# Kernel tuning notes

Measured on AMD Instinct MI355X. Metric: run time of the kernel, lower is better.

The kernel has to match this reference:

```python
import jax, jax.numpy as jnp
import numpy as np

EMBED_DIM = 1024
NUM_HEADS = 16
HEAD_DIM = EMBED_DIM // NUM_HEADS
WINDOW = 256
B, S = 2, 2048


def setup_inputs() -> dict:
    key = jax.random.key(0)
    ks = jax.random.split(key, 9)
    sc = 1.0 / np.sqrt(EMBED_DIM)
    inp = {
        "x": jax.random.normal(ks[0], (B, S, EMBED_DIM), dtype=jnp.float32),
        "Wq": jax.random.normal(ks[1], (EMBED_DIM, EMBED_DIM), dtype=jnp.float32) * sc,
        "Wk": jax.random.normal(ks[2], (EMBED_DIM, EMBED_DIM), dtype=jnp.float32) * sc,
        "Wv": jax.random.normal(ks[3], (EMBED_DIM, EMBED_DIM), dtype=jnp.float32) * sc,
        "Wo": jax.random.normal(ks[4], (EMBED_DIM, EMBED_DIM), dtype=jnp.float32) * sc,
        "bq": jax.random.normal(ks[5], (EMBED_DIM,), dtype=jnp.float32) * 0.01,
        "bk": jax.random.normal(ks[6], (EMBED_DIM,), dtype=jnp.float32) * 0.01,
        "bv": jax.random.normal(ks[7], (EMBED_DIM,), dtype=jnp.float32) * 0.01,
        "bo": jax.random.normal(ks[8], (EMBED_DIM,), dtype=jnp.float32) * 0.01,
    }
    return inp


def _sliding_window_mask(seq_len: int) -> jnp.ndarray:
    # True where attention is NOT permitted (future or beyond window)
    idx = jnp.arange(seq_len)
    rel = idx[None, :] - idx[:, None]  # (S, S): key_pos - query_pos
    return (rel > 0) | (rel < -WINDOW)


def reference(x, Wq, Wk, Wv, Wo, bq, bk, bv, bo):
    Bx, Sx, E = x.shape
    H, D = NUM_HEADS, HEAD_DIM
    # projections (torch Linear: y = x @ W.T + b)
    q = (x @ Wq.T + bq).reshape(Bx, Sx, H, D).transpose(0, 2, 1, 3)  # (B,H,S,D)
    k = (x @ Wk.T + bk).reshape(Bx, Sx, H, D).transpose(0, 2, 1, 3)
    v = (x @ Wv.T + bv).reshape(Bx, Sx, H, D).transpose(0, 2, 1, 3)
    q = q * (D ** -0.5)
    attn = jnp.einsum("bhqd,bhkd->bhqk", q, k)  # (B,H,S,S) dense scores
    mask = _sliding_window_mask(Sx)
    attn = jnp.where(mask, -jnp.inf, attn)
    attn = jax.nn.softmax(attn, axis=-1)
    y = jnp.einsum("bhqk,bhkd->bhqd", attn, v)
    y = y.transpose(0, 2, 1, 3).reshape(Bx, Sx, E)
    return y @ Wo.T + bo
```

## Files before the change

### kernel.cpp

```cpp
#include <hip/hip_runtime.h>

#define E_DIM 1024
#define NHEAD 16
#define HDIM 64
#define SEQ 2048
#define NBATCH 2
#define WIN 256
#define MTOK (NBATCH * SEQ)
#define BKT 32
#define NT (E_DIM / BKT)

typedef __attribute__((ext_vector_type(4))) float f32x4;
typedef __attribute__((ext_vector_type(8))) short short8;
typedef __attribute__((ext_vector_type(4))) unsigned short u16x4;

#define AS1 __attribute__((address_space(1)))
#define AS3 __attribute__((address_space(3)))

__device__ __forceinline__ void gll16(const void* g, void* l) {
    __builtin_amdgcn_global_load_lds((const AS1 void*)g, (AS3 void*)l, 16, 0, 0);
}

__device__ __forceinline__ unsigned short f2bf(float f) {
    union { float f; unsigned u; } a; a.f = f;
    unsigned r = a.u + 0x7fffu + ((a.u >> 16) & 1u);
    return (unsigned short)(r >> 16);
}

__global__ __launch_bounds__(256) void conv_f2b(const float* __restrict__ src,
                                                unsigned short* __restrict__ dst, int n4) {
    int i = blockIdx.x * 256 + threadIdx.x;
    int stride = gridDim.x * 256;
    for (; i < n4; i += stride) {
        float4 v = ((const float4*)src)[i];
        u16x4 o;
        o[0] = f2bf(v.x); o[1] = f2bf(v.y); o[2] = f2bf(v.z); o[3] = f2bf(v.w);
        ((u16x4*)dst)[i] = o;
    }
}

__global__ __launch_bounds__(256) void conv_w4(const float* __restrict__ w0, const float* __restrict__ w1,
                                               const float* __restrict__ w2, const float* __restrict__ w3,
                                               unsigned short* __restrict__ o0, unsigned short* __restrict__ o1,
                                               unsigned short* __restrict__ o2, unsigned short* __restrict__ o3) {
    const int m = blockIdx.y;
    const float* src = (m == 0) ? w0 : (m == 1) ? w1 : (m == 2) ? w2 : w3;
    unsigned short* dst = (m == 0) ? o0 : (m == 1) ? o1 : (m == 2) ? o2 : o3;
    int i = blockIdx.x * 256 + threadIdx.x;
    float4 v = ((const float4*)src)[i];
    u16x4 o;
    o[0] = f2bf(v.x); o[1] = f2bf(v.y); o[2] = f2bf(v.z); o[3] = f2bf(v.w);
    ((u16x4*)dst)[i] = o;
}

__global__ __launch_bounds__(512, 2) void gemm8_qkv(const unsigned short* __restrict__ xb,
        const unsigned short* __restrict__ wqb, const unsigned short* __restrict__ wkb,
        const unsigned short* __restrict__ wvb,
        const float* __restrict__ bq, const float* __restrict__ bk, const float* __restrict__ bv,
        unsigned short* __restrict__ qo, unsigned short* __restrict__ ko,
        unsigned short* __restrict__ vTo) {
    __shared__ char lds[131072];
    const int tid = threadIdx.x;
    const int w = tid >> 6, l = tid & 63;
    const int r16 = l & 15, kq = l >> 4;
    const int wm = w >> 2, wn = w & 3;
    const int m0 = blockIdx.x * 256;
    const int by = blockIdx.y;
    const int mat = by >> 2;
    const int nb = (by & 3) * 256;
    const unsigned short* Bw = (mat == 0) ? wqb : (mat == 1) ? wkb : wvb;

    const int srow = tid >> 2;
    const int sslot = tid & 3;
    const int fsw = (srow >> 1) & 3;
    const int gslot = (sslot ^ fsw) * 8;
    const unsigned short* aSrc0 = xb + (size_t)(m0 + srow) * E_DIM + gslot;
    const unsigned short* aSrc1 = aSrc0 + (size_t)128 * E_DIM;
    const unsigned short* bSrc0 = Bw + (size_t)(nb + srow) * E_DIM + gslot;
    const unsigned short* bSrc1 = bSrc0 + (size_t)128 * E_DIM;
    const int dstOff = w * 1024;

#define STAGE_A(t) { char* d_ = lds + ((t) & 3) * 32768 + dstOff; \
                     gll16(aSrc0 + (t) * BKT, d_); gll16(aSrc1 + (t) * BKT, d_ + 8192); }
#define STAGE_B(t) { char* d_ = lds + ((t) & 3) * 32768 + 16384 + dstOff; \
                     gll16(bSrc0 + (t) * BKT, d_); gll16(bSrc1 + (t) * BKT, d_ + 8192); }

    f32x4 acc[8][4];
    #pragma unroll
    for (int m = 0; m < 8; ++m)
        #pragma unroll
        for (int n = 0; n < 4; ++n)
            acc[m][n] = (f32x4){0.f, 0.f, 0.f, 0.f};

    STAGE_A(0); STAGE_B(0); STAGE_A(1); STAGE_B(1);

    const int fs = (r16 >> 1) & 3;
    const int rdoff = (kq ^ fs) * 16;

    for (int t = 0; t < NT; ++t) {
        if (t < NT - 1) { asm volatile("s_waitcnt vmcnt(4)" ::: "memory"); }
        else            { asm volatile("s_waitcnt vmcnt(0)" ::: "memory"); }
        __builtin_amdgcn_sched_barrier(0);
        __builtin_amdgcn_s_barrier();
        __builtin_amdgcn_sched_barrier(0);
        char* la = lds + (t & 3) * 32768;
        char* lb = la + 16384;
        short8 bfr[4], af[4];
        #pragma unroll
        for (int n = 0; n < 4; ++n)
            bfr[n] = *(const short8*)(lb + (wn * 64 + n * 16 + r16) * 64 + rdoff);
        #pragma unroll
        for (int j = 0; j < 4; ++j)
            af[j] = *(const short8*)(la + (wm * 128 + j * 16 + r16) * 64 + rdoff);
        if (t + 2 < NT) STAGE_A(t + 2);
        __builtin_amdgcn_s_barrier();
        __builtin_amdgcn_sched_barrier(0);
        __builtin_amdgcn_s_setprio(1);
        #pragma unroll
        for (int j = 0; j < 4; ++j)
            #pragma unroll
            for (int n = 0; n < 4; ++n)
                acc[j][n] = __builtin_amdgcn_mfma_f32_16x16x32_bf16(af[j], bfr[n], acc[j][n], 0, 0, 0);
        __builtin_amdgcn_s_setprio(0);
        short8 af2[4];
        #pragma unroll
        for (int j = 0; j < 4; ++j)
            af2[j] = *(const short8*)(la + (wm * 128 + (4 + j) * 16 + r16) * 64 + rdoff);
        if (t + 2 < NT) STAGE_B(t + 2);
        __builtin_amdgcn_s_barrier();
        __builtin_amdgcn_sched_barrier(0);
        __builtin_amdgcn_s_setprio(1);
        #pragma unroll
        for (int j = 0; j < 4; ++j)
            #pragma unroll
            for (int n = 0; n < 4; ++n)
                acc[4 + j][n] = __builtin_amdgcn_mfma_f32_16x16x32_bf16(af2[j], bfr[n], acc[4 + j][n], 0, 0, 0);
        __builtin_amdgcn_s_setprio(0);
    }
#undef STAGE_A
#undef STAGE_B

    const float* bias = (mat == 0) ? bq : (mat == 1) ? bk : bv;
    const float scale = (mat == 0) ? 0.125f : 1.0f;
    #pragma unroll
    for (int n = 0; n < 4; ++n) {
        int e = nb + wn * 64 + n * 16 + r16;
        float bb = bias[e];
        int h = e >> 6, d = e & 63;
        #pragma unroll
        for (int m = 0; m < 8; ++m) {
            int tok = m0 + wm * 128 + m * 16 + kq * 4;
            int b = tok >> 11, s = tok & (SEQ - 1);
            if (mat == 2) {
                u16x4 o;
                #pragma unroll
                for (int r = 0; r < 4; ++r) o[r] = f2bf(acc[m][n][r] + bb);
                *(u16x4*)(vTo + ((size_t)(b * NHEAD + h) * HDIM + d) * SEQ + s) = o;
            } else {
                unsigned short* dst = (mat == 0) ? qo : ko;
                #pragma unroll
                for (int r = 0; r < 4; ++r) {
                    float val = (acc[m][n][r] + bb) * scale;
                    dst[((size_t)(b * NHEAD + h) * SEQ + s + r) * HDIM + d] = f2bf(val);
                }
            }
        }
    }
}

__device__ __forceinline__ void gemm_tile(const unsigned short* __restrict__ A,
                                          const unsigned short* __restrict__ Bw,
                                          int m0, int n0,
                                          f32x4 acc[4][4], char* ldsA, char* ldsB) {
    const int t = threadIdx.x;
    const int w = t >> 6, l = t & 63;
    const int r16 = l & 15, kq = l >> 4;
    const int wr = w >> 1, wc = w & 1;
    const int srow = l >> 3, ps = l & 7;

    for (int kt = 0; kt < E_DIM / 64; ++kt) {
        #pragma unroll
        for (int c = 0; c < 4; ++c) {
            int chunk = w * 4 + c;
            int row = chunk * 8 + srow;
            int kslot = ps ^ (row & 7);
            gll16(A  + (size_t)(m0 + row) * E_DIM + kt * 64 + kslot * 8, ldsA + chunk * 1024);
            gll16(Bw + (size_t)(n0 + row) * E_DIM + kt * 64 + kslot * 8, ldsB + chunk * 1024);
        }
        __syncthreads();
        #pragma unroll
        for (int kk = 0; kk < 2; ++kk) {
            short8 af[4], bfr[4];
            #pragma unroll
            for (int m = 0; m < 4; ++m) {
                int rr = wr * 64 + m * 16 + r16;
                int c = kk * 4 + kq;
                af[m] = *(const short8*)(ldsA + rr * 128 + ((c ^ (rr & 7)) * 16));
            }
            #pragma unroll
            for (int n = 0; n < 4; ++n) {
                int rr = wc * 64 + n * 16 + r16;
                int c = kk * 4 + kq;
                bfr[n] = *(const short8*)(ldsB + rr * 128 + ((c ^ (rr & 7)) * 16));
            }
            #pragma unroll
            for (int m = 0; m < 4; ++m)
                #pragma unroll
                for (int n = 0; n < 4; ++n)
                    acc[m][n] = __builtin_amdgcn_mfma_f32_16x16x32_bf16(af[m], bfr[n], acc[m][n], 0, 0, 0);
        }
        __syncthreads();
    }
}

__global__ __launch_bounds__(256) void attn_swa(const unsigned short* __restrict__ q,
                                                const unsigned short* __restrict__ k,
                                                const unsigned short* __restrict__ vT,
                                                unsigned short* __restrict__ y) {
    __shared__ char plds[4 * 4096];
    const int t = threadIdx.x;
    const int w = t >> 6, l = t & 63;
    const int r16 = l & 15, kq = l >> 4;
    const int wid = blockIdx.x * 4 + w;
    const int bh = wid >> 6;
    const int q0 = (wid & 63) * 32;
    const unsigned short* qp = q + (size_t)bh * SEQ * HDIM;
    const unsigned short* kp = k + (size_t)bh * SEQ * HDIM;
    const unsigned short* vp = vT + (size_t)bh * HDIM * SEQ;
    char* pl = plds + w * 4096;

    short8 qf[2][2];
    #pragma unroll
    for (int mf = 0; mf < 2; ++mf) {
        const unsigned short* qr = qp + (q0 + mf * 16 + r16) * HDIM + kq * 8;
        qf[mf][0] = *(const short8*)(qr);
        qf[mf][1] = *(const short8*)(qr + 32);
    }

    f32x4 po[2][4];
    float mrow[2][4], lrow[2][4];
    #pragma unroll
    for (int mf = 0; mf < 2; ++mf) {
        #pragma unroll
        for (int nn = 0; nn < 4; ++nn) po[mf][nn] = (f32x4){0.f, 0.f, 0.f, 0.f};
        #pragma unroll
        for (int r = 0; r < 4; ++r) { mrow[mf][r] = -1e30f; lrow[mf][r] = 0.f; }
    }

    const int kstart = (q0 >= WIN) ? (q0 - WIN) : 0;
    for (int k0 = kstart; k0 <= q0 + 31; k0 += 32) {
        short8 kf[2][2];
        #pragma unroll
        for (int n = 0; n < 2; ++n) {
            const unsigned short* kr = kp + (size_t)(k0 + n * 16 + r16) * HDIM + kq * 8;
            kf[n][0] = *(const short8*)(kr);
            kf[n][1] = *(const short8*)(kr + 32);
        }
        f32x4 sc[2][2];
        #pragma unroll
        for (int mf = 0; mf < 2; ++mf)
            #pragma unroll
            for (int n = 0; n < 2; ++n) {
                f32x4 z = {0.f, 0.f, 0.f, 0.f};
                z = __builtin_amdgcn_mfma_f32_16x16x32_bf16(qf[mf][0], kf[n][0], z, 0, 0, 0);
                sc[mf][n] = __builtin_amdgcn_mfma_f32_16x16x32_bf16(qf[mf][1], kf[n][1], z, 0, 0, 0);
            }
        float tmax[2][4];
        #pragma unroll
        for (int mf = 0; mf < 2; ++mf)
            #pragma unroll
            for (int r = 0; r < 4; ++r) {
                int qrow = q0 + mf * 16 + kq * 4 + r;
                int key0 = k0 + r16;
                int key1 = key0 + 16;
                if (!(key0 <= qrow && key0 >= qrow - WIN)) sc[mf][0][r] = -1e30f;
                if (!(key1 <= qrow && key1 >= qrow - WIN)) sc[mf][1][r] = -1e30f;
                tmax[mf][r] = fmaxf(sc[mf][0][r], sc[mf][1][r]);
            }
        #pragma unroll
        for (int off = 1; off < 16; off <<= 1)
            #pragma unroll
            for (int mf = 0; mf < 2; ++mf)
                #pragma unroll
                for (int r = 0; r < 4; ++r)
                    tmax[mf][r] = fmaxf(tmax[mf][r], __shfl_xor(tmax[mf][r], off));
        float pv[2][2][4], psum[2][4];
        #pragma unroll
        for (int mf = 0; mf < 2; ++mf)
            #pragma unroll
            for (int r = 0; r < 4; ++r) {
                float mnew = fmaxf(mrow[mf][r], tmax[mf][r]);
                float resc = __expf(mrow[mf][r] - mnew);
                mrow[mf][r] = mnew;
                lrow[mf][r] *= resc;
                po[mf][0][r] *= resc; po[mf][1][r] *= resc;
                po[mf][2][r] *= resc; po[mf][3][r] *= resc;
                float p0 = (sc[mf][0][r] > -1e29f) ? __expf(sc[mf][0][r] - mnew) : 0.f;
                float p1 = (sc[mf][1][r] > -1e29f) ? __expf(sc[mf][1][r] - mnew) : 0.f;
                pv[mf][0][r] = p0; pv[mf][1][r] = p1;
                psum[mf][r] = p0 + p1;
            }
        #pragma unroll
        for (int off = 1; off < 16; off <<= 1)
            #pragma unroll
            for (int mf = 0; mf < 2; ++mf)
                #pragma unroll
                for (int r = 0; r < 4; ++r)
                    psum[mf][r] += __shfl_xor(psum[mf][r], off);
        #pragma unroll
        for (int mf = 0; mf < 2; ++mf)
            #pragma unroll
            for (int r = 0; r < 4; ++r) lrow[mf][r] += psum[mf][r];

        #pragma unroll
        for (int mf = 0; mf < 2; ++mf)
            #pragma unroll
            for (int r = 0; r < 4; ++r) {
                int row = kq * 4 + r;
                int c0 = r16 ^ ((row & 7) << 3);
                int c1 = (16 + r16) ^ ((row & 7) << 3);
                *(unsigned short*)(pl + mf * 2048 + row * 128 + c0 * 2) = f2bf(pv[mf][0][r]);
                *(unsigned short*)(pl + mf * 2048 + row * 128 + c1 * 2) = f2bf(pv[mf][1][r]);
            }
        short8 pa[2];
        #pragma unroll
        for (int mf = 0; mf < 2; ++mf)
            pa[mf] = *(const short8*)(pl + mf * 2048 + r16 * 128 + ((kq ^ (r16 & 7)) * 16));
        #pragma unroll
        for (int nn = 0; nn < 4; ++nn) {
            short8 vf = *(const short8*)(vp + (size_t)(nn * 16 + r16) * SEQ + k0 + kq * 8);
            po[0][nn] = __builtin_amdgcn_mfma_f32_16x16x32_bf16(pa[0], vf, po[0][nn], 0, 0, 0);
            po[1][nn] = __builtin_amdgcn_mfma_f32_16x16x32_bf16(pa[1], vf, po[1][nn], 0, 0, 0);
        }
    }

    const int b = bh >> 4, h = bh & 15;
    #pragma unroll
    for (int mf = 0; mf < 2; ++mf)
        #pragma unroll
        for (int nn = 0; nn < 4; ++nn)
            #pragma unroll
            for (int r = 0; r < 4; ++r) {
                int s = q0 + mf * 16 + kq * 4 + r;
                float val = po[mf][nn][r] / lrow[mf][r];
                y[((size_t)(b * SEQ + s)) * E_DIM + h * HDIM + nn * 16 + r16] = f2bf(val);
            }
}

__global__ __launch_bounds__(256) void gemm_out(const unsigned short* __restrict__ yb,
        const unsigned short* __restrict__ wob, const float* __restrict__ bo,
        float* __restrict__ out) {
    __shared__ char lds[32768];
    const int m0 = blockIdx.x * 128;
    const int n0 = blockIdx.y * 128;
    f32x4 acc[4][4];
    #pragma unroll
    for (int m = 0; m < 4; ++m)
        #pragma unroll
        for (int n = 0; n < 4; ++n)
            acc[m][n] = (f32x4){0.f, 0.f, 0.f, 0.f};

    gemm_tile(yb, wob, m0, n0, acc, lds, lds + 16384);

    const int t = threadIdx.x;
    const int w = t >> 6, l = t & 63;
    const int r16 = l & 15, kq = l >> 4;
    const int wr = w >> 1, wc = w & 1;
    #pragma unroll
    for (int n = 0; n < 4; ++n) {
        int e = n0 + wc * 64 + n * 16 + r16;
        float bb = bo[e];
        #pragma unroll
        for (int m = 0; m < 4; ++m) {
            #pragma unroll
            for (int r = 0; r < 4; ++r) {
                int tok = m0 + wr * 64 + m * 16 + kq * 4 + r;
                out[(size_t)tok * E_DIM + e] = acc[m][n][r] + bb;
            }
        }
    }
}

extern "C" void kernel_launch(void* const* d_in, const int* in_sizes, int n_in,
                              void* d_out, int out_size, void* d_ws, size_t ws_size,
                              hipStream_t stream) {
    const float* x  = (const float*)d_in[0];
    const float* Wq = (const float*)d_in[1];
    const float* Wk = (const float*)d_in[2];
    const float* Wv = (const float*)d_in[3];
    const float* Wo = (const float*)d_in[4];
    const float* bq = (const float*)d_in[5];
    const float* bk = (const float*)d_in[6];
    const float* bv = (const float*)d_in[7];
    const float* bo = (const float*)d_in[8];
    float* out = (float*)d_out;

    char* ws = (char*)d_ws;
    unsigned short* xb  = (unsigned short*)(ws);
    unsigned short* wqb = (unsigned short*)(ws + ((size_t)8 << 20));
    unsigned short* wkb = (unsigned short*)(ws + ((size_t)10 << 20));
    unsigned short* wvb = (unsigned short*)(ws + ((size_t)12 << 20));
    unsigned short* wob = (unsigned short*)(ws + ((size_t)14 << 20));
    unsigned short* qw  = (unsigned short*)(ws + ((size_t)16 << 20));
    unsigned short* kw  = (unsigned short*)(ws + ((size_t)24 << 20));
    unsigned short* vTw = (unsigned short*)(ws + ((size_t)40 << 20));
    unsigned short* yw  = (unsigned short*)(ws + ((size_t)48 << 20));

    conv_f2b<<<4096, 256, 0, stream>>>(x, xb, MTOK * E_DIM / 4);
    conv_w4<<<dim3(1024, 4), 256, 0, stream>>>(Wq, Wk, Wv, Wo, wqb, wkb, wvb, wob);

    gemm8_qkv<<<dim3(16, 12), 512, 0, stream>>>(xb, wqb, wkb, wvb, bq, bk, bv, qw, kw, vTw);
    attn_swa<<<512, 256, 0, stream>>>(qw, kw, vTw, yw);
    gemm_out<<<dim3(32, 8), 256, 0, stream>>>(yw, wob, bo, out);
}
```

Baseline: 177.3 us.

## Merge conversion kernels, simplify QKV GEMM loop, pipeline output GEMM

Merges the x and weight fp32-to-bf16 conversion kernels into a single launch with eight segments. The QKV GEMM's main loop now loads all eight A fragments at once and issues both stage loads together, dropping one barrier per iteration. The output projection GEMM gets the same 4-stage global_load_lds pipeline with BK=32, XOR swizzle and 2 blocks per CU. This is meant to cut launch overhead, barrier stalls and exposed load latency, at the cost of more registers held for fragments.

After: 166.1 us. 1.07x faster.

```diff
diff --git a/kernel.cpp b/kernel.cpp
--- a/kernel.cpp
+++ b/kernel.cpp
@@ -27,25 +27,20 @@
     return (unsigned short)(r >> 16);
 }
 
-__global__ __launch_bounds__(256) void conv_f2b(const float* __restrict__ src,
-                                                unsigned short* __restrict__ dst, int n4) {
-    int i = blockIdx.x * 256 + threadIdx.x;
-    int stride = gridDim.x * 256;
-    for (; i < n4; i += stride) {
-        float4 v = ((const float4*)src)[i];
-        u16x4 o;
-        o[0] = f2bf(v.x); o[1] = f2bf(v.y); o[2] = f2bf(v.z); o[3] = f2bf(v.w);
-        ((u16x4*)dst)[i] = o;
-    }
-}
-
-__global__ __launch_bounds__(256) void conv_w4(const float* __restrict__ w0, const float* __restrict__ w1,
-                                               const float* __restrict__ w2, const float* __restrict__ w3,
-                                               unsigned short* __restrict__ o0, unsigned short* __restrict__ o1,
-                                               unsigned short* __restrict__ o2, unsigned short* __restrict__ o3) {
-    const int m = blockIdx.y;
-    const float* src = (m == 0) ? w0 : (m == 1) ? w1 : (m == 2) ? w2 : w3;
-    unsigned short* dst = (m == 0) ? o0 : (m == 1) ? o1 : (m == 2) ? o2 : o3;
+__global__ __launch_bounds__(256) void conv_all(const float* __restrict__ x,
+        const float* __restrict__ w0, const float* __restrict__ w1,
+        const float* __restrict__ w2, const float* __restrict__ w3,
+        unsigned short* __restrict__ xo,
+        unsigned short* __restrict__ o0, unsigned short* __restrict__ o1,
+        unsigned short* __restrict__ o2, unsigned short* __restrict__ o3) {
+    const int seg = blockIdx.y;
+    const float* src;
+    unsigned short* dst;
+    if (seg < 4) { src = x + (size_t)seg * 1048576; dst = xo + (size_t)seg * 1048576; }
+    else {
+        src = (seg == 4) ? w0 : (seg == 5) ? w1 : (seg == 6) ? w2 : w3;
+        dst = (seg == 4) ? o0 : (seg == 5) ? o1 : (seg == 6) ? o2 : o3;
+    }
     int i = blockIdx.x * 256 + threadIdx.x;
     float4 v = ((const float4*)src)[i];
     u16x4 o;
@@ -105,36 +100,20 @@
         __builtin_amdgcn_sched_barrier(0);
         char* la = lds + (t & 3) * 32768;
         char* lb = la + 16384;
-        short8 bfr[4], af[4];
+        short8 bfr[4], af[8];
         #pragma unroll
         for (int n = 0; n < 4; ++n)
             bfr[n] = *(const short8*)(lb + (wn * 64 + n * 16 + r16) * 64 + rdoff);
         #pragma unroll
-        for (int j = 0; j < 4; ++j)
+        for (int j = 0; j < 8; ++j)
             af[j] = *(const short8*)(la + (wm * 128 + j * 16 + r16) * 64 + rdoff);
-        if (t + 2 < NT) STAGE_A(t + 2);
-        __builtin_amdgcn_s_barrier();
-        __builtin_amdgcn_sched_barrier(0);
+        if (t + 2 < NT) { STAGE_A(t + 2); STAGE_B(t + 2); }
         __builtin_amdgcn_s_setprio(1);
         #pragma unroll
-        for (int j = 0; j < 4; ++j)
+        for (int j = 0; j < 8; ++j)
             #pragma unroll
             for (int n = 0; n < 4; ++n)
                 acc[j][n] = __builtin_amdgcn_mfma_f32_16x16x32_bf16(af[j], bfr[n], acc[j][n], 0, 0, 0);
-        __builtin_amdgcn_s_setprio(0);
-        short8 af2[4];
-        #pragma unroll
-        for (int j = 0; j < 4; ++j)
-            af2[j] = *(const short8*)(la + (wm * 128 + (4 + j) * 16 + r16) * 64 + rdoff);
-        if (t + 2 < NT) STAGE_B(t + 2);
-        __builtin_amdgcn_s_barrier();
-        __builtin_amdgcn_sched_barrier(0);
-        __builtin_amdgcn_s_setprio(1);
-        #pragma unroll
-        for (int j = 0; j < 4; ++j)
-            #pragma unroll
-            for (int n = 0; n < 4; ++n)
-                acc[4 + j][n] = __builtin_amdgcn_mfma_f32_16x16x32_bf16(af2[j], bfr[n], acc[4 + j][n], 0, 0, 0);
         __builtin_amdgcn_s_setprio(0);
     }
 #undef STAGE_A
@@ -168,48 +147,83 @@
     }
 }
 
-__device__ __forceinline__ void gemm_tile(const unsigned short* __restrict__ A,
-                                          const unsigned short* __restrict__ Bw,
-                                          int m0, int n0,
-                                          f32x4 acc[4][4], char* ldsA, char* ldsB) {
-    const int t = threadIdx.x;
-    const int w = t >> 6, l = t & 63;
+__global__ __launch_bounds__(256, 2) void gemm_out(const unsigned short* __restrict__ yb,
+        const unsigned short* __restrict__ wob, const float* __restrict__ bo,
+        float* __restrict__ out) {
+    __shared__ char lds[65536];
+    const int tid = threadIdx.x;
+    const int w = tid >> 6, l = tid & 63;
     const int r16 = l & 15, kq = l >> 4;
     const int wr = w >> 1, wc = w & 1;
-    const int srow = l >> 3, ps = l & 7;
-
-    for (int kt = 0; kt < E_DIM / 64; ++kt) {
-        #pragma unroll
-        for (int c = 0; c < 4; ++c) {
-            int chunk = w * 4 + c;
-            int row = chunk * 8 + srow;
-            int kslot = ps ^ (row & 7);
-            gll16(A  + (size_t)(m0 + row) * E_DIM + kt * 64 + kslot * 8, ldsA + chunk * 1024);
-            gll16(Bw + (size_t)(n0 + row) * E_DIM + kt * 64 + kslot * 8, ldsB + chunk * 1024);
+    const int m0 = blockIdx.x * 128;
+    const int n0 = blockIdx.y * 128;
+
+    const int srow = tid >> 2;
+    const int sslot = tid & 3;
+    const int fsw = (srow >> 1) & 3;
+    const int gslot = (sslot ^ fsw) * 8;
+    const unsigned short* aSrc0 = yb + (size_t)(m0 + srow) * E_DIM + gslot;
+    const unsigned short* aSrc1 = aSrc0 + (size_t)64 * E_DIM;
+    const unsigned short* bSrc0 = wob + (size_t)(n0 + srow) * E_DIM + gslot;
+    const unsigned short* bSrc1 = bSrc0 + (size_t)64 * E_DIM;
+    const int dstOff = w * 1024;
+
+#define STAGE_A(t) { char* d_ = lds + ((t) & 3) * 16384 + dstOff; \
+                     gll16(aSrc0 + (t) * BKT, d_); gll16(aSrc1 + (t) * BKT, d_ + 4096); }
+#define STAGE_B(t) { char* d_ = lds + ((t) & 3) * 16384 + 8192 + dstOff; \
+                     gll16(bSrc0 + (t) * BKT, d_); gll16(bSrc1 + (t) * BKT, d_ + 4096); }
+
+    f32x4 acc[4][4];
+    #pragma unroll
+    for (int m = 0; m < 4; ++m)
+        #pragma unroll
+        for (int n = 0; n < 4; ++n)
+            acc[m][n] = (f32x4){0.f, 0.f, 0.f, 0.f};
+
+    STAGE_A(0); STAGE_B(0); STAGE_A(1); STAGE_B(1);
+
+    const int fs = (r16 >> 1) & 3;
+    const int rdoff = (kq ^ fs) * 16;
+
+    for (int t = 0; t < NT; ++t) {
+        if (t < NT - 1) { asm volatile("s_waitcnt vmcnt(4)" ::: "memory"); }
+        else            { asm volatile("s_waitcnt vmcnt(0)" ::: "memory"); }
+        __builtin_amdgcn_sched_barrier(0);
+        __builtin_amdgcn_s_barrier();
+        __builtin_amdgcn_sched_barrier(0);
+        char* la = lds + (t & 3) * 16384;
+        char* lb = la + 8192;
+        short8 bfr[4], af[4];
+        #pragma unroll
+        for (int n = 0; n < 4; ++n)
+            bfr[n] = *(const short8*)(lb + (wc * 64 + n * 16 + r16) * 64 + rdoff);
+        #pragma unroll
+        for (int m = 0; m < 4; ++m)
+            af[m] = *(const short8*)(la + (wr * 64 + m * 16 + r16) * 64 + rdoff);
+        if (t + 2 < NT) { STAGE_A(t + 2); STAGE_B(t + 2); }
+        __builtin_amdgcn_s_setprio(1);
+        #pragma unroll
+        for (int m = 0; m < 4; ++m)
+            #pragma unroll
+            for (int n = 0; n < 4; ++n)
+                acc[m][n] = __builtin_amdgcn_mfma_f32_16x16x32_bf16(af[m], bfr[n], acc[m][n], 0, 0, 0);
+        __builtin_amdgcn_s_setprio(0);
+    }
+#undef STAGE_A
+#undef STAGE_B
+
+    #pragma unroll
+    for (int n = 0; n < 4; ++n) {
+        int e = n0 + wc * 64 + n * 16 + r16;
+        float bb = bo[e];
+        #pragma unroll
+        for (int m = 0; m < 4; ++m) {
+            #pragma unroll
+            for (int r = 0; r < 4; ++r) {
+                int tok = m0 + wr * 64 + m * 16 + kq * 4 + r;
+                out[(size_t)tok * E_DIM + e] = acc[m][n][r] + bb;
+            }
         }
-        __syncthreads();
-        #pragma unroll
-        for (int kk = 0; kk < 2; ++kk) {
-            short8 af[4], bfr[4];
-            #pragma unroll
-            for (int m = 0; m < 4; ++m) {
-                int rr = wr * 64 + m * 16 + r16;
-                int c = kk * 4 + kq;
-                af[m] = *(const short8*)(ldsA + rr * 128 + ((c ^ (rr & 7)) * 16));
-            }
-            #pragma unroll
-            for (int n = 0; n < 4; ++n) {
-                int rr = wc * 64 + n * 16 + r16;
-                int c = kk * 4 + kq;
-                bfr[n] = *(const short8*)(ldsB + rr * 128 + ((c ^ (rr & 7)) * 16));
-            }
-            #pragma unroll
-            for (int m = 0; m < 4; ++m)
-                #pragma unroll
-                for (int n = 0; n < 4; ++n)
-                    acc[m][n] = __builtin_amdgcn_mfma_f32_16x16x32_bf16(af[m], bfr[n], acc[m][n], 0, 0, 0);
-        }
-        __syncthreads();
     }
 }
 
@@ -347,40 +361,6 @@
             }
 }
 
-__global__ __launch_bounds__(256) void gemm_out(const unsigned short* __restrict__ yb,
-        const unsigned short* __restrict__ wob, const float* __restrict__ bo,
-        float* __restrict__ out) {
-    __shared__ char lds[32768];
-    const int m0 = blockIdx.x * 128;
-    const int n0 = blockIdx.y * 128;
-    f32x4 acc[4][4];
-    #pragma unroll
-    for (int m = 0; m < 4; ++m)
-        #pragma unroll
-        for (int n = 0; n < 4; ++n)
-            acc[m][n] = (f32x4){0.f, 0.f, 0.f, 0.f};
-
-    gemm_tile(yb, wob, m0, n0, acc, lds, lds + 16384);
-
-    const int t = threadIdx.x;
-    const int w = t >> 6, l = t & 63;
-    const int r16 = l & 15, kq = l >> 4;
-    const int wr = w >> 1, wc = w & 1;
-    #pragma unroll
-    for (int n = 0; n < 4; ++n) {
-        int e = n0 + wc * 64 + n * 16 + r16;
-        float bb = bo[e];
-        #pragma unroll
-        for (int m = 0; m < 4; ++m) {
-            #pragma unroll
-            for (int r = 0; r < 4; ++r) {
-                int tok = m0 + wr * 64 + m * 16 + kq * 4 + r;
-                out[(size_t)tok * E_DIM + e] = acc[m][n][r] + bb;
-            }
-        }
-    }
-}
-
 extern "C" void kernel_launch(void* const* d_in, const int* in_sizes, int n_in,
                               void* d_out, int out_size, void* d_ws, size_t ws_size,
                               hipStream_t stream) {
@@ -406,8 +386,7 @@
     unsigned short* vTw = (unsigned short*)(ws + ((size_t)40 << 20));
     unsigned short* yw  = (unsigned short*)(ws + ((size_t)48 << 20));
 
-    conv_f2b<<<4096, 256, 0, stream>>>(x, xb, MTOK * E_DIM / 4);
-    conv_w4<<<dim3(1024, 4), 256, 0, stream>>>(Wq, Wk, Wv, Wo, wqb, wkb, wvb, wob);
+    conv_all<<<dim3(1024, 8), 256, 0, stream>>>(x, Wq, Wk, Wv, Wo, xb, wqb, wkb, wvb, wob);
 
     gemm8_qkv<<<dim3(16, 12), 512, 0, stream>>>(xb, wqb, wkb, wvb, bq, bk, bv, qw, kw, vTw);
     attn_swa<<<512, 256, 0, stream>>>(qw, kw, vTw, yw);
```
